# Kernel tuning notes

Measured on AMD Instinct MI355X. Metric: run time of the kernel, lower is better.

## Reference

```python
import jax, jax.numpy as jnp
import numpy as np
from functools import partial

DN = ('NCHW', 'OIHW', 'NCHW')


def dwise_conv(x, pw, dw):
    # pointwise 1x1 conv then depthwise 3x3 conv (pad 1), no bias
    c = pw.shape[0]
    h = jax.lax.conv_general_dilated(x, pw, (1, 1), 'VALID', dimension_numbers=DN)
    return jax.lax.conv_general_dilated(h, dw, (1, 1), ((1, 1), (1, 1)),
                                        dimension_numbers=DN, feature_group_count=c)


def l2norm(t, eps=1e-12):
    # torch F.normalize(dim=-1): x / max(||x||_2, eps)
    n = jnp.sqrt(jnp.sum(t * t, axis=-1, keepdims=True))
    return t / jnp.maximum(n, eps)


def cross_attention(x, y, z, temperature, q_pw, q_dw, k_pw, k_dw, v_pw, v_dw, proj_w, num_heads=3):
    b, c, h, w = x.shape
    hc = c // num_heads  # per-head channels
    q = x + dwise_conv(x, q_pw, q_dw)
    k = y + dwise_conv(y, k_pw, k_dw)
    v = z + dwise_conv(z, v_pw, v_dw)
    # b (head hc) h w -> b head hc (h w)
    q = q.reshape(b, num_heads, hc, h * w)
    k = k.reshape(b, num_heads, hc, h * w)
    v = v.reshape(b, num_heads, hc, h * w)
    q = l2norm(q)
    k = l2norm(k)
    # transposed attention: small hc x hc score per head
    attn = jnp.einsum('bhcn,bhdn->bhcd', q, k) * temperature  # temperature broadcasts (head,1,1)
    attn = jax.nn.softmax(attn, axis=-1)
    out = jnp.einsum('bhcd,bhdn->bhcn', attn, v)
    out = out.reshape(b, c, h, w)
    return jax.lax.conv_general_dilated(out, proj_w, (1, 1), 'VALID', dimension_numbers=DN)


def setup_inputs() -> dict:
    key = jax.random.key(0)
    ks = jax.random.split(key, 12)
    B, C, H, W, HEADS = 8, 96, 192, 192, 3
    s = 0.05
    return {
        'x': jax.random.normal(ks[0], (B, C, H, W), jnp.float32),
        'y': jax.random.normal(ks[1], (B, C, H, W), jnp.float32),
        'z': jax.random.normal(ks[2], (B, C, H, W), jnp.float32),
        'temperature': jnp.ones((HEADS, 1, 1), jnp.float32),
        'q_pw': jax.random.normal(ks[3], (C, C, 1, 1), jnp.float32) * s,
        'q_dw': jax.random.normal(ks[4], (C, 1, 3, 3), jnp.float32) * s,
        'k_pw': jax.random.normal(ks[5], (C, C, 1, 1), jnp.float32) * s,
        'k_dw': jax.random.normal(ks[6], (C, 1, 3, 3), jnp.float32) * s,
        'v_pw': jax.random.normal(ks[7], (C, C, 1, 1), jnp.float32) * s,
        'v_dw': jax.random.normal(ks[8], (C, 1, 3, 3), jnp.float32) * s,
        'proj_w': jax.random.normal(ks[9], (C, C, 1, 1), jnp.float32) * s,
    }


def reference(x, y, z, temperature, q_pw, q_dw, k_pw, k_dw, v_pw, v_dw, proj_w):
    return cross_attention(x, y, z, temperature, q_pw, q_dw, k_pw, k_dw, v_pw, v_dw, proj_w, num_heads=3)
```

## Files before the change

kernel.cpp:

```cpp
#include <hip/hip_runtime.h>


#define B_  8
#define C_  96
#define W_  192
#define HW_ 36864
#define NB_ 32

typedef __attribute__((ext_vector_type(8)))  short short8;
typedef __attribute__((ext_vector_type(4)))  float f32x4;
typedef __attribute__((ext_vector_type(16))) float f32x16;

__device__ __forceinline__ unsigned short f2b(float f){
  unsigned u = __float_as_uint(f);
  u += 0x7fffu + ((u >> 16) & 1u);
  return (unsigned short)(u >> 16);
}
__device__ __forceinline__ float blo(unsigned u){ return __uint_as_float(u << 16); }
__device__ __forceinline__ float bhi(unsigned u){ return __uint_as_float(u & 0xffff0000u); }

__device__ __forceinline__ void barrier_lds(){
  asm volatile("s_waitcnt lgkmcnt(0)\n\ts_barrier" ::: "memory");
}

template<int NORM>
__global__ __launch_bounds__(512, 1)
void k_conv(const float* __restrict__ xsrc, const float* __restrict__ pw,
            const float* __restrict__ dwt, unsigned short* __restrict__ outq,
            float* __restrict__ nrm)
{
  __shared__ unsigned short xrow[192 * 104];
  __shared__ unsigned short hring[3][96 * 196];

  const int t = threadIdx.x, lane = t & 63, wv = t >> 6;
  const int band = blockIdx.x, b = blockIdx.y;
  const int r0 = band * 6;
  const int l15 = lane & 15, l4 = lane >> 4;
  const int mtg = wv >> 2, ntg = wv & 3;
  const float* xb = xsrc + (size_t)b * C_ * HW_;

  int scp[5], spg[5];
  #pragma unroll
  for (int i = 0; i < 5; ++i){
    const int idx = i * 512 + t;
    scp[i] = idx / 48; spg[i] = idx - scp[i] * 48;
  }

  short8 afrag[3][3];
  #pragma unroll
  for (int mt = 0; mt < 3; ++mt){
    #pragma unroll
    for (int ks = 0; ks < 3; ++ks){
      const int m = mtg * 48 + mt * 16 + l15;
      const float* ap = pw + m * 96 + ks * 32 + l4 * 8;
      const float4 f0 = *(const float4*)ap;
      const float4 f1 = *(const float4*)(ap + 4);
      union { short8 v; unsigned short u[8]; } tmp;
      tmp.u[0]=f2b(f0.x); tmp.u[1]=f2b(f0.y); tmp.u[2]=f2b(f0.z); tmp.u[3]=f2b(f0.w);
      tmp.u[4]=f2b(f1.x); tmp.u[5]=f2b(f1.y); tmp.u[6]=f2b(f1.z); tmp.u[7]=f2b(f1.w);
      afrag[mt][ks] = tmp.v;
    }
  }

  {
    uint4* p = (uint4*)&hring[0][0];
    for (int i = t; i < 7056; i += 512) p[i] = make_uint4(0,0,0,0);
  }

  float ssq[12];
  #pragma unroll
  for (int i = 0; i < 12; ++i) ssq[i] = 0.f;

  auto stage_write = [&](const float4* fa, const float4* fb){
    #pragma unroll
    for (int i = 0; i < 5; ++i){
      if (scp[i] < 48){
        const int pg = spg[i];
        const unsigned pk0 = (unsigned)f2b(fa[i].x) | ((unsigned)f2b(fb[i].x) << 16);
        const unsigned pk1 = (unsigned)f2b(fa[i].y) | ((unsigned)f2b(fb[i].y) << 16);
        const unsigned pk2 = (unsigned)f2b(fa[i].z) | ((unsigned)f2b(fb[i].z) << 16);
        const unsigned pk3 = (unsigned)f2b(fa[i].w) | ((unsigned)f2b(fb[i].w) << 16);
        const int s = (pg >> 1) & 3;
        const unsigned a0 = (s & 1) ? pk1 : pk0;
        const unsigned a1 = (s & 1) ? pk0 : pk1;
        const unsigned a2 = (s & 1) ? pk3 : pk2;
        const unsigned a3 = (s & 1) ? pk2 : pk3;
        const unsigned q0 = (s & 2) ? a2 : a0;
        const unsigned q1 = (s & 2) ? a3 : a1;
        const unsigned q2 = (s & 2) ? a0 : a2;
        const unsigned q3 = (s & 2) ? a1 : a3;
        unsigned short* basep = xrow + (4*pg) * 104 + 2*scp[i];
        *(unsigned*)(basep + ((0 ^ s) * 104)) = q0;
        *(unsigned*)(basep + ((1 ^ s) * 104)) = q1;
        *(unsigned*)(basep + ((2 ^ s) * 104)) = q2;
        *(unsigned*)(basep + ((3 ^ s) * 104)) = q3;
      }
    }
  };
  auto stage_load = [&](int rs, float4* fa, float4* fb){
    #pragma unroll
    for (int i = 0; i < 5; ++i){
      if (scp[i] < 48){
        const float* xp = xb + (size_t)(2*scp[i]) * HW_ + (size_t)rs * W_ + 4*spg[i];
        fa[i] = *(const float4*)xp;
        fb[i] = *(const float4*)(xp + HW_);
      }
    }
  };

  if (r0 - 1 >= 0){
    float4 fa[5], fb[5];
    stage_load(r0 - 1, fa, fb);
    stage_write(fa, fb);
  }
  barrier_lds();

  #pragma unroll 1
  for (int r = r0 - 1; r <= r0 + 6; ++r){
    const int slot = (r + 3) % 3;
    const int rs = r + 1;
    const bool do_stage = (rs <= r0 + 6) && (rs < 192);
    float4 sfa[5], sfb[5];
    if (do_stage) stage_load(rs, sfa, sfb);

    if (r >= 0 && r < 192){
      f32x4 acc[3][3];
      #pragma unroll
      for (int mt = 0; mt < 3; ++mt)
        #pragma unroll
        for (int nt = 0; nt < 3; ++nt){
          acc[mt][nt][0]=0.f; acc[mt][nt][1]=0.f; acc[mt][nt][2]=0.f; acc[mt][nt][3]=0.f;
        }
      #pragma unroll
      for (int ks = 0; ks < 3; ++ks){
        #pragma unroll
        for (int nt = 0; nt < 3; ++nt){
          const short8 bv = *(const short8*)(xrow + (ntg*48 + nt*16 + l15) * 104 + ks*32 + l4*8);
          #pragma unroll
          for (int mt = 0; mt < 3; ++mt)
            acc[mt][nt] = __builtin_amdgcn_mfma_f32_16x16x32_bf16(afrag[mt][ks], bv, acc[mt][nt], 0, 0, 0);
        }
      }
      unsigned short* hs = &hring[slot][0];
      #pragma unroll
      for (int mt = 0; mt < 3; ++mt)
        #pragma unroll
        for (int nt = 0; nt < 3; ++nt)
          #pragma unroll
          for (int reg = 0; reg < 4; ++reg){
            const int m = mtg*48 + mt*16 + l4*4 + reg;
            const int n = ntg*48 + nt*16 + l15;
            hs[m * 196 + 1 + n] = f2b(acc[mt][nt][reg]);
          }
    } else {
      uint4* p = (uint4*)&hring[slot][0];
      for (int i = t; i < 2352; i += 512) p[i] = make_uint4(0,0,0,0);
    }
    barrier_lds();

    if (do_stage) stage_write(sfa, sfb);
    if (r - 1 >= r0){
      const int rr = r - 1;
      const unsigned short* h0 = &hring[(rr + 2) % 3][0];
      const unsigned short* h1 = &hring[(rr + 3) % 3][0];
      const unsigned short* h2 = &hring[(rr + 4) % 3][0];
      if (lane < 48){
        const int g = lane;
        float4 xr_[12];
        const float* xrp = xb + (size_t)rr * W_ + 4*g;
        #pragma unroll
        for (int cc = 0; cc < 12; ++cc)
          xr_[cc] = *(const float4*)(xrp + (size_t)(wv * 12 + cc) * HW_);
        #pragma unroll
        for (int cc = 0; cc < 12; ++cc){
          const int chs = __builtin_amdgcn_readfirstlane(wv * 12 + cc);
          float wgt[9];
          #pragma unroll
          for (int i = 0; i < 9; ++i) wgt[i] = dwt[chs * 9 + i];
          const int rb = chs * 196 + 4 * g;
          float hv[3][6];
          {
            const unsigned short* hp[3] = {h0 + rb, h1 + rb, h2 + rb};
            #pragma unroll
            for (int d = 0; d < 3; ++d){
              const uint2 ua = *(const uint2*)(hp[d]);
              const unsigned ub = *(const unsigned*)(hp[d] + 4);
              hv[d][0]=blo(ua.x); hv[d][1]=bhi(ua.x); hv[d][2]=blo(ua.y);
              hv[d][3]=bhi(ua.y); hv[d][4]=blo(ub);   hv[d][5]=bhi(ub);
            }
          }
          float o[4] = {xr_[cc].x, xr_[cc].y, xr_[cc].z, xr_[cc].w};
          #pragma unroll
          for (int j = 0; j < 4; ++j){
            float s = o[j];
            #pragma unroll
            for (int d = 0; d < 3; ++d){
              s = fmaf(wgt[d*3+0], hv[d][j],   s);
              s = fmaf(wgt[d*3+1], hv[d][j+1], s);
              s = fmaf(wgt[d*3+2], hv[d][j+2], s);
            }
            o[j] = s;
            if (NORM) ssq[cc] = fmaf(s, s, ssq[cc]);
          }
          const size_t cb = (size_t)(b * C_ + chs) * HW_ + (size_t)rr * W_ + 4*g;
          const unsigned p0 = (unsigned)f2b(o[0]) | ((unsigned)f2b(o[1]) << 16);
          const unsigned p1 = (unsigned)f2b(o[2]) | ((unsigned)f2b(o[3]) << 16);
          *(uint2*)(outq + cb) = make_uint2(p0, p1);
        }
      }
    }
    barrier_lds();
  }

  if (NORM){
    #pragma unroll
    for (int cc = 0; cc < 12; ++cc){
      float s = ssq[cc];
      #pragma unroll
      for (int off = 32; off; off >>= 1) s += __shfl_xor(s, off);
      if (lane == 0)
        nrm[((size_t)b * NB_ + band) * C_ + wv * 12 + cc] = s;
    }
  }
}

__global__ __launch_bounds__(256, 2)
void k_gemm(const unsigned short* __restrict__ Bsrc, const float* __restrict__ Asrc,
            float* __restrict__ Dst)
{
  __shared__ unsigned short xT[256 * 104];
  __shared__ unsigned short aw[96 * 104];
  const int t = threadIdx.x;
  const int b = blockIdx.y;
  const int p0 = blockIdx.x * 256;
  const int lane = t & 63, w = t >> 6;
  const int l15 = lane & 15, l4 = lane >> 4;

  const float* Ab = Asrc + b * C_ * C_;
  #pragma unroll
  for (int j = 0; j < 18; ++j){
    const int pi = j * 256 + t;
    const int row = pi / 48, c2 = (pi - row * 48) * 2;
    const float a0 = Ab[row * 96 + c2], a1 = Ab[row * 96 + c2 + 1];
    *(unsigned*)(aw + row * 104 + c2) = (unsigned)f2b(a0) | ((unsigned)f2b(a1) << 16);
  }
  #pragma unroll 1
  for (int i = 0; i < 12; ++i){
    const int idx = i * 256 + t;
    const int cp = idx >> 6, pg = idx & 63;
    const unsigned short* vp = Bsrc + (size_t)b * C_ * HW_ + (size_t)(2*cp) * HW_ + p0 + 4*pg;
    const uint2 ua = *(const uint2*)vp;
    const uint2 ub = *(const uint2*)(vp + HW_);
    const unsigned pk0 = (ua.x & 0xffffu) | (ub.x << 16);
    const unsigned pk1 = (ua.x >> 16)     | (ub.x & 0xffff0000u);
    const unsigned pk2 = (ua.y & 0xffffu) | (ub.y << 16);
    const unsigned pk3 = (ua.y >> 16)     | (ub.y & 0xffff0000u);
    const int s = (pg >> 1) & 3;
    const unsigned a0 = (s & 1) ? pk1 : pk0;
    const unsigned a1 = (s & 1) ? pk0 : pk1;
    const unsigned a2 = (s & 1) ? pk3 : pk2;
    const unsigned a3 = (s & 1) ? pk2 : pk3;
    const unsigned q0 = (s & 2) ? a2 : a0;
    const unsigned q1 = (s & 2) ? a3 : a1;
    const unsigned q2 = (s & 2) ? a0 : a2;
    const unsigned q3 = (s & 2) ? a1 : a3;
    unsigned short* basep = xT + (4*pg) * 104 + 2*cp;
    *(unsigned*)(basep + ((0 ^ s) * 104)) = q0;
    *(unsigned*)(basep + ((1 ^ s) * 104)) = q1;
    *(unsigned*)(basep + ((2 ^ s) * 104)) = q2;
    *(unsigned*)(basep + ((3 ^ s) * 104)) = q3;
  }
  __syncthreads();

  f32x4 acc[6][4];
  #pragma unroll
  for (int i = 0; i < 6; ++i)
    #pragma unroll
    for (int j = 0; j < 4; ++j){ acc[i][j][0]=0.f; acc[i][j][1]=0.f; acc[i][j][2]=0.f; acc[i][j][3]=0.f; }

  #pragma unroll
  for (int ks = 0; ks < 3; ++ks){
    short8 a[6];
    #pragma unroll
    for (int mt = 0; mt < 6; ++mt)
      a[mt] = *(const short8*)(aw + (mt * 16 + l15) * 104 + ks * 32 + l4 * 8);
    #pragma unroll
    for (int nt = 0; nt < 4; ++nt){
      const short8 bv = *(const short8*)(xT + (w * 64 + nt * 16 + l15) * 104 + ks * 32 + l4 * 8);
      #pragma unroll
      for (int mt = 0; mt < 6; ++mt)
        acc[mt][nt] = __builtin_amdgcn_mfma_f32_16x16x32_bf16(a[mt], bv, acc[mt][nt], 0, 0, 0);
    }
  }

  float* D = Dst + (size_t)b * C_ * HW_ + p0;
  #pragma unroll
  for (int mt = 0; mt < 6; ++mt)
    #pragma unroll
    for (int nt = 0; nt < 4; ++nt)
      #pragma unroll
      for (int r = 0; r < 4; ++r)
        D[(size_t)(mt * 16 + l4 * 4 + r) * HW_ + w * 64 + nt * 16 + l15] = acc[mt][nt][r];
}

__global__ __launch_bounds__(256, 2)
void k_gram(const unsigned short* __restrict__ qb, const unsigned short* __restrict__ kb,
            float* __restrict__ Gp)
{
  __shared__ unsigned short pan[2][32 * 520];
  const int t = threadIdx.x, lane = t & 63, w = t >> 6;
  const int ns = blockIdx.x, bh = blockIdx.y;
  const int b = bh / 3, h = bh - b * 3;
  const size_t base = ((size_t)b * C_ + h * 32) * HW_ + ns * 1536;
  const int l31 = lane & 31, l5 = lane >> 5;

  f32x16 acc;
  #pragma unroll
  for (int r = 0; r < 16; ++r) acc[r] = 0.f;

  #pragma unroll 1
  for (int rd = 0; rd < 3; ++rd){
    __syncthreads();
    #pragma unroll 8
    for (int j = 0; j < 64; ++j){
      const int idx = j * 256 + t;
      const int op = idx >> 13;
      const int rem = idx & 8191;
      const int ch = rem >> 8, dcol = rem & 255;
      const unsigned* src = (const unsigned*)((op ? kb : qb) + base + (size_t)ch * HW_ + rd * 512) + dcol;
      *(unsigned*)(&pan[op][ch * 520 + dcol * 2]) = *src;
    }
    __syncthreads();
    #pragma unroll
    for (int j8 = 0; j8 < 8; ++j8){
      const int s = j8 * 4 + w;
      const short8 av = *(const short8*)(&pan[0][l31 * 520 + s * 16 + l5 * 8]);
      const short8 bv = *(const short8*)(&pan[1][l31 * 520 + s * 16 + l5 * 8]);
      acc = __builtin_amdgcn_mfma_f32_32x32x16_bf16(av, bv, acc, 0, 0, 0);
    }
  }
  __syncthreads();
  float* red = (float*)pan;
  #pragma unroll
  for (int r = 0; r < 16; ++r) red[w * 1024 + r * 64 + lane] = acc[r];
  __syncthreads();
  #pragma unroll
  for (int q = 0; q < 4; ++q){
    const int fi = q * 256 + t;
    const float v = red[fi] + red[1024 + fi] + red[2048 + fi] + red[3072 + fi];
    const int rr = fi >> 6, ll = fi & 63;
    const int c = (rr & 3) + 8 * (rr >> 2) + 4 * (ll >> 5);
    const int d = ll & 31;
    Gp[(((size_t)ns * 24 + bh) * 32 + c) * 32 + d] = v;
  }
}

__global__ __launch_bounds__(256)
void k_attn(const float* __restrict__ Gp, const float* __restrict__ qqp,
            const float* __restrict__ kkp, const float* __restrict__ temp,
            const float* __restrict__ proj, float* __restrict__ M)
{
  const int b = blockIdx.x, t = threadIdx.x;
  __shared__ float at[3][32][32];
  __shared__ float ninv[2][C_];
  if (t < 2 * C_){
    const int kind = t / C_, r = t - kind * C_;
    const float* P = kind ? kkp : qqp;
    float s = 0.f;
    #pragma unroll
    for (int ns = 0; ns < NB_; ++ns) s += P[((size_t)b * NB_ + ns) * C_ + r];
    ninv[kind][r] = 1.f / fmaxf(sqrtf(s), 1e-12f);
  }
  __syncthreads();
  for (int idx = t; idx < 3 * 1024; idx += 256){
    const int h = idx >> 10, rem = idx & 1023, cc = rem >> 5, dd = rem & 31;
    float g = 0.f;
    #pragma unroll
    for (int ns = 0; ns < 24; ++ns)
      g += Gp[(((size_t)ns * 24 + b * 3 + h) * 32 + cc) * 32 + dd];
    at[h][cc][dd] = g * ninv[0][h * 32 + cc] * ninv[1][h * 32 + dd] * temp[h];
  }
  __syncthreads();
  if (t < C_){
    const int h = t >> 5, cc = t & 31;
    float m = -1e30f;
    for (int dd = 0; dd < 32; ++dd) m = fmaxf(m, at[h][cc][dd]);
    float s = 0.f;
    for (int dd = 0; dd < 32; ++dd){ const float e = expf(at[h][cc][dd] - m); at[h][cc][dd] = e; s += e; }
    const float inv = 1.f / s;
    for (int dd = 0; dd < 32; ++dd) at[h][cc][dd] *= inv;
  }
  __syncthreads();
  for (int idx = t; idx < C_ * C_; idx += 256){
    const int o = idx / 96, hd = idx - o * 96, h = hd >> 5, dd = hd & 31;
    float m = 0.f;
    #pragma unroll
    for (int cc = 0; cc < 32; ++cc)
      m = fmaf(proj[o * 96 + h * 32 + cc], at[h][cc][dd], m);
    M[(size_t)b * 9216 + idx] = m;
  }
}

extern "C" void kernel_launch(void* const* d_in, const int* in_sizes, int n_in,
                              void* d_out, int out_size, void* d_ws, size_t ws_size,
                              hipStream_t stream)
{
  const float* x     = (const float*)d_in[0];
  const float* y     = (const float*)d_in[1];
  const float* z     = (const float*)d_in[2];
  const float* temp  = (const float*)d_in[3];
  const float* q_pwc = (const float*)d_in[4];
  const float* q_dwc = (const float*)d_in[5];
  const float* k_pwc = (const float*)d_in[6];
  const float* k_dwc = (const float*)d_in[7];
  const float* v_pwc = (const float*)d_in[8];
  const float* v_dwc = (const float*)d_in[9];
  const float* proj  = (const float*)d_in[10];

  char* ws = (char*)d_ws;
  unsigned short* qb = (unsigned short*)(ws + 56623104);
  unsigned short* kb = (unsigned short*)(ws + 113246208);
  unsigned short* vb = (unsigned short*)(ws + 169869312);
  float* qqp = (float*)(ws + 226492416);
  float* kkp = (float*)(ws + 226590720);
  float* Gp  = (float*)(ws + 4194304);
  float* M   = (float*)(ws + 8388608);
  float* out = (float*)d_out;

  const dim3 gc(NB_, B_);
  k_conv<1><<<gc, 512, 0, stream>>>(x, q_pwc, q_dwc, qb, qqp);
  k_conv<1><<<gc, 512, 0, stream>>>(y, k_pwc, k_dwc, kb, kkp);
  k_conv<0><<<gc, 512, 0, stream>>>(z, v_pwc, v_dwc, vb, nullptr);
  k_gram<<<dim3(24, 24), 256, 0, stream>>>(qb, kb, Gp);
  k_attn<<<B_, 256, 0, stream>>>(Gp, qqp, kkp, temp, proj, M);
  k_gemm<<<dim3(HW_ / 256, B_), 256, 0, stream>>>(vb, M, out);
}
```

Measured before the change: 313.6 us.

## Merge q/k/v conv launches into one 3D-grid kernel with 768-thread blocks

Replaces three separate conv launches with a single launch whose z-dimension selects the q, k or v input, weights and outputs. Block size grows from 512 to 768 threads (12 waves). Each wave now computes one 16-row M tile across 96 columns instead of a 48x48 tile, and handles 8 channels in the depthwise stage. The merge removes launch gaps and tail effects between the three convs, and the extra waves aim to hide latency better. The trade-off is less A-fragment reuse per wave and a norm accumulation that now also runs for v, where its result is discarded.

```diff
diff --git a/kernel.cpp b/kernel.cpp
--- a/kernel.cpp
+++ b/kernel.cpp
@@ -23,93 +23,97 @@
   asm volatile("s_waitcnt lgkmcnt(0)\n\ts_barrier" ::: "memory");
 }
 
-template<int NORM>
-__global__ __launch_bounds__(512, 1)
-void k_conv(const float* __restrict__ xsrc, const float* __restrict__ pw,
-            const float* __restrict__ dwt, unsigned short* __restrict__ outq,
-            float* __restrict__ nrm)
+__global__ __launch_bounds__(768, 1)
+void k_conv_all(const float* __restrict__ x0, const float* __restrict__ x1,
+                const float* __restrict__ x2,
+                const float* __restrict__ pw0, const float* __restrict__ pw1,
+                const float* __restrict__ pw2,
+                const float* __restrict__ dw0, const float* __restrict__ dw1,
+                const float* __restrict__ dw2,
+                unsigned short* __restrict__ o0, unsigned short* __restrict__ o1,
+                unsigned short* __restrict__ o2,
+                float* __restrict__ n0, float* __restrict__ n1)
 {
   __shared__ unsigned short xrow[192 * 104];
   __shared__ unsigned short hring[3][96 * 196];
 
   const int t = threadIdx.x, lane = t & 63, wv = t >> 6;
-  const int band = blockIdx.x, b = blockIdx.y;
+  const int band = blockIdx.x, b = blockIdx.y, cid = blockIdx.z;
+  const float* xsrc = (cid == 0) ? x0 : (cid == 1) ? x1 : x2;
+  const float* pw   = (cid == 0) ? pw0 : (cid == 1) ? pw1 : pw2;
+  const float* dwt  = (cid == 0) ? dw0 : (cid == 1) ? dw1 : dw2;
+  unsigned short* outq = (cid == 0) ? o0 : (cid == 1) ? o1 : o2;
+  float* nrm = (cid == 0) ? n0 : (cid == 1) ? n1 : nullptr;
+
   const int r0 = band * 6;
   const int l15 = lane & 15, l4 = lane >> 4;
-  const int mtg = wv >> 2, ntg = wv & 3;
+  const int mtg = wv % 6, ntg = wv / 6;
   const float* xb = xsrc + (size_t)b * C_ * HW_;
 
-  int scp[5], spg[5];
-  #pragma unroll
-  for (int i = 0; i < 5; ++i){
-    const int idx = i * 512 + t;
+  int scp[3], spg[3];
+  #pragma unroll
+  for (int i = 0; i < 3; ++i){
+    const int idx = i * 768 + t;
     scp[i] = idx / 48; spg[i] = idx - scp[i] * 48;
   }
 
-  short8 afrag[3][3];
-  #pragma unroll
-  for (int mt = 0; mt < 3; ++mt){
-    #pragma unroll
-    for (int ks = 0; ks < 3; ++ks){
-      const int m = mtg * 48 + mt * 16 + l15;
-      const float* ap = pw + m * 96 + ks * 32 + l4 * 8;
-      const float4 f0 = *(const float4*)ap;
-      const float4 f1 = *(const float4*)(ap + 4);
-      union { short8 v; unsigned short u[8]; } tmp;
-      tmp.u[0]=f2b(f0.x); tmp.u[1]=f2b(f0.y); tmp.u[2]=f2b(f0.z); tmp.u[3]=f2b(f0.w);
-      tmp.u[4]=f2b(f1.x); tmp.u[5]=f2b(f1.y); tmp.u[6]=f2b(f1.z); tmp.u[7]=f2b(f1.w);
-      afrag[mt][ks] = tmp.v;
-    }
+  short8 afrag[3];
+  #pragma unroll
+  for (int ks = 0; ks < 3; ++ks){
+    const int m = mtg * 16 + l15;
+    const float* ap = pw + m * 96 + ks * 32 + l4 * 8;
+    const float4 f0 = *(const float4*)ap;
+    const float4 f1 = *(const float4*)(ap + 4);
+    union { short8 v; unsigned short u[8]; } tmp;
+    tmp.u[0]=f2b(f0.x); tmp.u[1]=f2b(f0.y); tmp.u[2]=f2b(f0.z); tmp.u[3]=f2b(f0.w);
+    tmp.u[4]=f2b(f1.x); tmp.u[5]=f2b(f1.y); tmp.u[6]=f2b(f1.z); tmp.u[7]=f2b(f1.w);
+    afrag[ks] = tmp.v;
   }
 
   {
     uint4* p = (uint4*)&hring[0][0];
-    for (int i = t; i < 7056; i += 512) p[i] = make_uint4(0,0,0,0);
-  }
-
-  float ssq[12];
-  #pragma unroll
-  for (int i = 0; i < 12; ++i) ssq[i] = 0.f;
+    for (int i = t; i < 7056; i += 768) p[i] = make_uint4(0,0,0,0);
+  }
+
+  float ssq[8];
+  #pragma unroll
+  for (int i = 0; i < 8; ++i) ssq[i] = 0.f;
 
   auto stage_write = [&](const float4* fa, const float4* fb){
     #pragma unroll
-    for (int i = 0; i < 5; ++i){
-      if (scp[i] < 48){
-        const int pg = spg[i];
-        const unsigned pk0 = (unsigned)f2b(fa[i].x) | ((unsigned)f2b(fb[i].x) << 16);
-        const unsigned pk1 = (unsigned)f2b(fa[i].y) | ((unsigned)f2b(fb[i].y) << 16);
-        const unsigned pk2 = (unsigned)f2b(fa[i].z) | ((unsigned)f2b(fb[i].z) << 16);
-        const unsigned pk3 = (unsigned)f2b(fa[i].w) | ((unsigned)f2b(fb[i].w) << 16);
-        const int s = (pg >> 1) & 3;
-        const unsigned a0 = (s & 1) ? pk1 : pk0;
-        const unsigned a1 = (s & 1) ? pk0 : pk1;
-        const unsigned a2 = (s & 1) ? pk3 : pk2;
-        const unsigned a3 = (s & 1) ? pk2 : pk3;
-        const unsigned q0 = (s & 2) ? a2 : a0;
-        const unsigned q1 = (s & 2) ? a3 : a1;
-        const unsigned q2 = (s & 2) ? a0 : a2;
-        const unsigned q3 = (s & 2) ? a1 : a3;
-        unsigned short* basep = xrow + (4*pg) * 104 + 2*scp[i];
-        *(unsigned*)(basep + ((0 ^ s) * 104)) = q0;
-        *(unsigned*)(basep + ((1 ^ s) * 104)) = q1;
-        *(unsigned*)(basep + ((2 ^ s) * 104)) = q2;
-        *(unsigned*)(basep + ((3 ^ s) * 104)) = q3;
-      }
+    for (int i = 0; i < 3; ++i){
+      const int pg = spg[i];
+      const unsigned pk0 = (unsigned)f2b(fa[i].x) | ((unsigned)f2b(fb[i].x) << 16);
+      const unsigned pk1 = (unsigned)f2b(fa[i].y) | ((unsigned)f2b(fb[i].y) << 16);
+      const unsigned pk2 = (unsigned)f2b(fa[i].z) | ((unsigned)f2b(fb[i].z) << 16);
+      const unsigned pk3 = (unsigned)f2b(fa[i].w) | ((unsigned)f2b(fb[i].w) << 16);
+      const int s = (pg >> 1) & 3;
+      const unsigned a0 = (s & 1) ? pk1 : pk0;
+      const unsigned a1 = (s & 1) ? pk0 : pk1;
+      const unsigned a2 = (s & 1) ? pk3 : pk2;
+      const unsigned a3 = (s & 1) ? pk2 : pk3;
+      const unsigned q0 = (s & 2) ? a2 : a0;
+      const unsigned q1 = (s & 2) ? a3 : a1;
+      const unsigned q2 = (s & 2) ? a0 : a2;
+      const unsigned q3 = (s & 2) ? a1 : a3;
+      unsigned short* basep = xrow + (4*pg) * 104 + 2*scp[i];
+      *(unsigned*)(basep + ((0 ^ s) * 104)) = q0;
+      *(unsigned*)(basep + ((1 ^ s) * 104)) = q1;
+      *(unsigned*)(basep + ((2 ^ s) * 104)) = q2;
+      *(unsigned*)(basep + ((3 ^ s) * 104)) = q3;
     }
   };
   auto stage_load = [&](int rs, float4* fa, float4* fb){
     #pragma unroll
-    for (int i = 0; i < 5; ++i){
-      if (scp[i] < 48){
-        const float* xp = xb + (size_t)(2*scp[i]) * HW_ + (size_t)rs * W_ + 4*spg[i];
-        fa[i] = *(const float4*)xp;
-        fb[i] = *(const float4*)(xp + HW_);
-      }
+    for (int i = 0; i < 3; ++i){
+      const float* xp = xb + (size_t)(2*scp[i]) * HW_ + (size_t)rs * W_ + 4*spg[i];
+      fa[i] = *(const float4*)xp;
+      fb[i] = *(const float4*)(xp + HW_);
     }
   };
 
   if (r0 - 1 >= 0){
-    float4 fa[5], fb[5];
+    float4 fa[3], fb[3];
     stage_load(r0 - 1, fa, fb);
     stage_write(fa, fb);
   }
@@ -120,41 +124,35 @@
     const int slot = (r + 3) % 3;
     const int rs = r + 1;
     const bool do_stage = (rs <= r0 + 6) && (rs < 192);
-    float4 sfa[5], sfb[5];
+    float4 sfa[3], sfb[3];
     if (do_stage) stage_load(rs, sfa, sfb);
 
     if (r >= 0 && r < 192){
-      f32x4 acc[3][3];
-      #pragma unroll
-      for (int mt = 0; mt < 3; ++mt)
-        #pragma unroll
-        for (int nt = 0; nt < 3; ++nt){
-          acc[mt][nt][0]=0.f; acc[mt][nt][1]=0.f; acc[mt][nt][2]=0.f; acc[mt][nt][3]=0.f;
-        }
+      f32x4 acc[6];
+      #pragma unroll
+      for (int nt = 0; nt < 6; ++nt){
+        acc[nt][0]=0.f; acc[nt][1]=0.f; acc[nt][2]=0.f; acc[nt][3]=0.f;
+      }
       #pragma unroll
       for (int ks = 0; ks < 3; ++ks){
         #pragma unroll
-        for (int nt = 0; nt < 3; ++nt){
-          const short8 bv = *(const short8*)(xrow + (ntg*48 + nt*16 + l15) * 104 + ks*32 + l4*8);
-          #pragma unroll
-          for (int mt = 0; mt < 3; ++mt)
-            acc[mt][nt] = __builtin_amdgcn_mfma_f32_16x16x32_bf16(afrag[mt][ks], bv, acc[mt][nt], 0, 0, 0);
+        for (int nt = 0; nt < 6; ++nt){
+          const short8 bv = *(const short8*)(xrow + (ntg*96 + nt*16 + l15) * 104 + ks*32 + l4*8);
+          acc[nt] = __builtin_amdgcn_mfma_f32_16x16x32_bf16(afrag[ks], bv, acc[nt], 0, 0, 0);
         }
       }
       unsigned short* hs = &hring[slot][0];
       #pragma unroll
-      for (int mt = 0; mt < 3; ++mt)
+      for (int nt = 0; nt < 6; ++nt)
         #pragma unroll
-        for (int nt = 0; nt < 3; ++nt)
-          #pragma unroll
-          for (int reg = 0; reg < 4; ++reg){
-            const int m = mtg*48 + mt*16 + l4*4 + reg;
-            const int n = ntg*48 + nt*16 + l15;
-            hs[m * 196 + 1 + n] = f2b(acc[mt][nt][reg]);
-          }
+        for (int reg = 0; reg < 4; ++reg){
+          const int m = mtg*16 + l4*4 + reg;
+          const int n = ntg*96 + nt*16 + l15;
+          hs[m * 196 + 1 + n] = f2b(acc[nt][reg]);
+        }
     } else {
       uint4* p = (uint4*)&hring[slot][0];
-      for (int i = t; i < 2352; i += 512) p[i] = make_uint4(0,0,0,0);
+      for (int i = t; i < 2352; i += 768) p[i] = make_uint4(0,0,0,0);
     }
     barrier_lds();
 
@@ -166,14 +164,14 @@
       const unsigned short* h2 = &hring[(rr + 4) % 3][0];
       if (lane < 48){
         const int g = lane;
-        float4 xr_[12];
+        float4 xr_[8];
         const float* xrp = xb + (size_t)rr * W_ + 4*g;
         #pragma unroll
-        for (int cc = 0; cc < 12; ++cc)
-          xr_[cc] = *(const float4*)(xrp + (size_t)(wv * 12 + cc) * HW_);
+        for (int cc = 0; cc < 8; ++cc)
+          xr_[cc] = *(const float4*)(xrp + (size_t)(wv * 8 + cc) * HW_);
         #pragma unroll
-        for (int cc = 0; cc < 12; ++cc){
-          const int chs = __builtin_amdgcn_readfirstlane(wv * 12 + cc);
+        for (int cc = 0; cc < 8; ++cc){
+          const int chs = __builtin_amdgcn_readfirstlane(wv * 8 + cc);
           float wgt[9];
           #pragma unroll
           for (int i = 0; i < 9; ++i) wgt[i] = dwt[chs * 9 + i];
@@ -200,7 +198,7 @@
               s = fmaf(wgt[d*3+2], hv[d][j+2], s);
             }
             o[j] = s;
-            if (NORM) ssq[cc] = fmaf(s, s, ssq[cc]);
+            ssq[cc] = fmaf(s, s, ssq[cc]);
           }
           const size_t cb = (size_t)(b * C_ + chs) * HW_ + (size_t)rr * W_ + 4*g;
           const unsigned p0 = (unsigned)f2b(o[0]) | ((unsigned)f2b(o[1]) << 16);
@@ -212,14 +210,14 @@
     barrier_lds();
   }
 
-  if (NORM){
-    #pragma unroll
-    for (int cc = 0; cc < 12; ++cc){
+  if (nrm){
+    #pragma unroll
+    for (int cc = 0; cc < 8; ++cc){
       float s = ssq[cc];
       #pragma unroll
       for (int off = 32; off; off >>= 1) s += __shfl_xor(s, off);
       if (lane == 0)
-        nrm[((size_t)b * NB_ + band) * C_ + wv * 12 + cc] = s;
+        nrm[((size_t)b * NB_ + band) * C_ + wv * 8 + cc] = s;
     }
   }
 }
@@ -427,10 +425,8 @@
   float* M   = (float*)(ws + 8388608);
   float* out = (float*)d_out;
 
-  const dim3 gc(NB_, B_);
-  k_conv<1><<<gc, 512, 0, stream>>>(x, q_pwc, q_dwc, qb, qqp);
-  k_conv<1><<<gc, 512, 0, stream>>>(y, k_pwc, k_dwc, kb, kkp);
-  k_conv<0><<<gc, 512, 0, stream>>>(z, v_pwc, v_dwc, vb, nullptr);
+  k_conv_all<<<dim3(NB_, B_, 3), 768, 0, stream>>>(
+      x, y, z, q_pwc, k_pwc, v_pwc, q_dwc, k_dwc, v_dwc, qb, kb, vb, qqp, kkp);
   k_gram<<<dim3(24, 24), 256, 0, stream>>>(qb, kb, Gp);
   k_attn<<<B_, 256, 0, stream>>>(Gp, qqp, kkp, temp, proj, M);
   k_gemm<<<dim3(HW_ / 256, B_), 256, 0, stream>>>(vb, M, out);
```

Measured after the change: 281.5 us (median of 2 runs). 1.11x faster.
